# Kernel tuning notes

Measured on AMD Instinct MI355X. Metric: run time of the kernel, lower is better.

Reference implementation:

```python
import jax, jax.numpy as jnp
import numpy as np
import math

D = 2048
NH = 16       # query heads
NKV = 4       # kv heads (GQA)
HD = 128
SOFTCLAMP = 50.0
ROPE_BASE = 10000.0
B = 4
SQ_VLM = 1024
SQ_ACT = 64
S_CACHE = 256


def _heads(x, n):
    # [B,S,n*HD] -> [B,n,S,HD]
    b, s, _ = x.shape
    return x.reshape(b, s, n, HD).transpose(0, 2, 1, 3)


def _rope_cos_sin(pos):
    # pos: [B,S] int -> cos,sin [B,1,S,HD]
    inv_freq = 1.0 / (ROPE_BASE ** (jnp.arange(0, HD, 2, dtype=jnp.float32) / HD))
    freqs = pos.astype(jnp.float32)[..., None] * inv_freq  # [B,S,HD/2]
    emb = jnp.concatenate([freqs, freqs], axis=-1)         # [B,S,HD]
    return jnp.cos(emb)[:, None], jnp.sin(emb)[:, None]


def _apply_rope(x, cos, sin):
    # x: [B,H,S,HD]
    x1, x2 = x[..., : HD // 2], x[..., HD // 2 :]
    rot = jnp.concatenate([-x2, x1], axis=-1)
    return x * cos + rot * sin


def setup_inputs() -> dict:
    key = jax.random.key(0)
    ks = jax.random.split(key, 16)
    sc = lambda d: 1.0 / math.sqrt(d)
    inp = {
        'attention_mask': jnp.zeros((B, 1, SQ_VLM + SQ_ACT, S_CACHE + SQ_VLM + SQ_ACT), jnp.float32),
        'pos_vlm': jnp.broadcast_to(jnp.arange(S_CACHE, S_CACHE + SQ_VLM, dtype=jnp.int32), (B, SQ_VLM)),
        'pos_action': jnp.broadcast_to(jnp.arange(S_CACHE + SQ_VLM, S_CACHE + SQ_VLM + SQ_ACT, dtype=jnp.int32), (B, SQ_ACT)),
        'h_vlm': jax.random.normal(ks[0], (B, SQ_VLM, D), jnp.float32),
        'h_action': jax.random.normal(ks[1], (B, SQ_ACT, D), jnp.float32),
        'k_cache': jax.random.normal(ks[2], (B, NKV, S_CACHE, HD), jnp.float32),
        'v_cache': jax.random.normal(ks[3], (B, NKV, S_CACHE, HD), jnp.float32),
        'Wq_vlm': jax.random.normal(ks[4], (D, NH * HD), jnp.float32) * sc(D),
        'Wk_vlm': jax.random.normal(ks[5], (D, NKV * HD), jnp.float32) * sc(D),
        'Wv_vlm': jax.random.normal(ks[6], (D, NKV * HD), jnp.float32) * sc(D),
        'Wq_act': jax.random.normal(ks[7], (D, NH * HD), jnp.float32) * sc(D),
        'Wk_act': jax.random.normal(ks[8], (D, NKV * HD), jnp.float32) * sc(D),
        'Wv_act': jax.random.normal(ks[9], (D, NKV * HD), jnp.float32) * sc(D),
        'Wo_act': jax.random.normal(ks[10], (NH * HD, D), jnp.float32) * sc(NH * HD),
    }
    return inp


def reference(attention_mask, pos_vlm, pos_action, h_vlm, h_action, k_cache, v_cache,
              Wq_vlm, Wk_vlm, Wv_vlm, Wq_act, Wk_act, Wv_act, Wo_act):
    group = NH // NKV

    def qkv(h, pos, Wq, Wk, Wv):
        q = _heads(h @ Wq, NH)
        k = _heads(h @ Wk, NKV)
        v = _heads(h @ Wv, NKV)
        cos, sin = _rope_cos_sin(pos)
        return _apply_rope(q, cos, sin), _apply_rope(k, cos, sin), v

    q_v, k_v, v_v = qkv(h_vlm, pos_vlm, Wq_vlm, Wk_vlm, Wv_vlm)
    q_a, k_a, v_a = qkv(h_action, pos_action, Wq_act, Wk_act, Wv_act)

    # repeat_kv (GQA) on every KV source, cached mixture first (append_non_active order)
    rep = lambda t: jnp.repeat(t, group, axis=1)  # [B,NKV,S,HD] -> [B,NH,S,HD]
    k = jnp.concatenate([rep(k_cache), rep(k_v), rep(k_a)], axis=2)
    v = jnp.concatenate([rep(v_cache), rep(v_v), rep(v_a)], axis=2)
    q = jnp.concatenate([q_v, q_a], axis=2)  # [B,NH,Sq,HD]

    scores = jnp.einsum('bhqd,bhkd->bhqk', q, k) / math.sqrt(HD)
    scores = jnp.tanh(scores / SOFTCLAMP) * SOFTCLAMP + attention_mask
    w = jax.nn.softmax(scores.astype(jnp.float32), axis=-1).astype(q.dtype)
    out = jnp.einsum('bhqk,bhkd->bhqd', w, v)
    out = out.transpose(0, 2, 1, 3).reshape(B, SQ_VLM + SQ_ACT, NH * HD)

    # split by q_lens; 'vlm' is in post_attn_skip_names -> no o_proj, dropped
    out_action = out[:, SQ_VLM:, :]
    return out_action @ Wo_act
```

## Files before the change

### kernel.cpp

```cpp
#include <hip/hip_runtime.h>
#include <cmath>

#define NH 16
#define NKV 4
#define HD 128
#define DMODEL 2048
#define BB 4
#define SQV 1024
#define SQA 64
#define SCACHE 256
#define STOT 1344
#define SQTOT 1088
#define NSPLIT 7

typedef unsigned short u16;
typedef __attribute__((ext_vector_type(8))) short short8;
typedef __attribute__((ext_vector_type(4))) float f32x4;

__device__ __forceinline__ float b2f(u16 u) {
    union { float f; unsigned int i; } x; x.i = ((unsigned int)u) << 16; return x.f;
}
__device__ __forceinline__ u16 f2b(float f) {
    unsigned int x = __float_as_uint(f);
    x = x + 0x7fffu + ((x >> 16) & 1u);
    return (u16)(x >> 16);
}

__device__ __forceinline__ void gload16(const void* g, void* l) {
    __builtin_amdgcn_global_load_lds((const __attribute__((address_space(1))) void*)g,
                                     (__attribute__((address_space(3))) void*)l, 16, 0, 0);
}

__device__ __forceinline__ void transpose_body(const float* in, u16* out, int N,
                                               int bx, int by) {
    __shared__ __align__(16) u16 t[64 * 66];
    int n0 = bx * 64, k0 = by * 64;
    int tid = threadIdx.x;
    int r = tid >> 3;
    int c8 = (tid & 7) * 8;
#pragma unroll
    for (int h = 0; h < 2; h++) {
        int k = r + h * 32;
        const float* f = in + (size_t)(k0 + k) * N + n0 + c8;
        float4 a = *(const float4*)f, b = *(const float4*)(f + 4);
        u16 vv[8] = {f2b(a.x), f2b(a.y), f2b(a.z), f2b(a.w),
                     f2b(b.x), f2b(b.y), f2b(b.z), f2b(b.w)};
#pragma unroll
        for (int j = 0; j < 8; j++) t[(c8 + j) * 66 + k] = vv[j];
    }
    __syncthreads();
#pragma unroll
    for (int h = 0; h < 2; h++) {
        int n = r + h * 32;
        short8 v;
#pragma unroll
        for (int j = 0; j < 8; j++) ((u16*)&v)[j] = t[n * 66 + c8 + j];
        *(short8*)(out + (size_t)(n0 + n) * 2048 + k0 + c8) = v;
    }
}

__device__ __forceinline__ void transpose_vc(const float* vc, u16* VT, int idx) {
    __shared__ __align__(16) u16 tv[64 * 66];
    int bkv = idx >> 3, t8 = idx & 7;
    int key0 = (t8 >> 1) * 64, d0 = (t8 & 1) * 64;
    const float* in = vc + ((size_t)bkv * SCACHE + key0) * HD + d0;
    u16* out = VT + ((size_t)bkv * HD + d0) * STOT + key0;
    int tid = threadIdx.x;
    int r = tid >> 3, c8 = (tid & 7) * 8;
#pragma unroll
    for (int h = 0; h < 2; h++) {
        int k = r + h * 32;
        const float* f = in + (size_t)k * HD + c8;
        float4 a = *(const float4*)f, b = *(const float4*)(f + 4);
        u16 vv[8] = {f2b(a.x), f2b(a.y), f2b(a.z), f2b(a.w),
                     f2b(b.x), f2b(b.y), f2b(b.z), f2b(b.w)};
#pragma unroll
        for (int j = 0; j < 8; j++) tv[(c8 + j) * 66 + k] = vv[j];
    }
    __syncthreads();
#pragma unroll
    for (int h = 0; h < 2; h++) {
        int d = r + h * 32;
        short8 v;
#pragma unroll
        for (int j = 0; j < 8; j++) ((u16*)&v)[j] = tv[d * 66 + c8 + j];
        *(short8*)(out + (size_t)d * STOT + c8) = v;
    }
}

__global__ void k_prep(const float* __restrict__ mask,
                       const float* __restrict__ kc, const float* __restrict__ vc,
                       const float* __restrict__ hv, const float* __restrict__ ha,
                       const float* __restrict__ w0, u16* __restrict__ o0,
                       const float* __restrict__ w1, u16* __restrict__ o1,
                       const float* __restrict__ w2, u16* __restrict__ o2,
                       const float* __restrict__ w3, u16* __restrict__ o3,
                       const float* __restrict__ w4, u16* __restrict__ o4,
                       const float* __restrict__ w5, u16* __restrict__ o5,
                       float* __restrict__ cosT, float* __restrict__ sinT,
                       u16* __restrict__ maskS, u16* __restrict__ K_all, u16* __restrict__ VT_all,
                       u16* __restrict__ hv16, u16* __restrict__ ha16) {
    int gx = blockIdx.x, tid = threadIdx.x;
    if (gx < 3072) {
        if (gx < 256)        transpose_body(w0, o0, 512,  gx & 7,  gx >> 3);
        else if (gx < 512)   { int g = gx - 256;  transpose_body(w1, o1, 512,  g & 7,  g >> 3); }
        else if (gx < 768)   { int g = gx - 512;  transpose_body(w2, o2, 512,  g & 7,  g >> 3); }
        else if (gx < 1024)  { int g = gx - 768;  transpose_body(w3, o3, 512,  g & 7,  g >> 3); }
        else if (gx < 2048)  { int g = gx - 1024; transpose_body(w4, o4, 2048, g & 31, g >> 5); }
        else                 { int g = gx - 2048; transpose_body(w5, o5, 2048, g & 31, g >> 5); }
        return;
    }
    int bx = gx - 3072;
    if (bx < 336) {
        int i = bx * 256 + tid;
        if (i < STOT * 64) {
            int p = i >> 6, j = i & 63;
            float inv = __expf(-(float)j * (9.210340371976184f / 64.0f));
            float ang = (float)p * inv;
            cosT[i] = cosf(ang);
            sinT[i] = sinf(ang);
        }
    } else if (bx < 1680) {
        int i = (bx - 336) * 256 + tid;
        int b = i / (SQA * STOT);
        int r = i % (SQA * STOT);
        size_t s = (size_t)b * SQTOT * STOT + (size_t)SQV * STOT + r;
        maskS[i] = f2b(mask[s]);
    } else if (bx < 1936) {
        int i = (bx - 1680) * 256 + tid;
        int e = i * 8;
        int bk = e / (SCACHE * HD);
        int off = e % (SCACHE * HD);
        size_t dst = (size_t)bk * STOT * HD + off;
        const float* fk = kc + e;
        u16 tk[8];
#pragma unroll
        for (int j = 0; j < 8; j++) tk[j] = f2b(fk[j]);
        *(short8*)(K_all + dst) = *(short8*)tk;
    } else if (bx < 6032) {
        int i = (bx - 1936) * 256 + tid;
        int e = i * 8;
        const float* f = hv + e;
        float4 a = *(const float4*)f, b = *(const float4*)(f + 4);
        u16 t[8] = {f2b(a.x), f2b(a.y), f2b(a.z), f2b(a.w),
                    f2b(b.x), f2b(b.y), f2b(b.z), f2b(b.w)};
        *(short8*)(hv16 + e) = *(short8*)t;
    } else if (bx < 6288) {
        int i = (bx - 6032) * 256 + tid;
        int e = i * 8;
        const float* f = ha + e;
        float4 a = *(const float4*)f, b = *(const float4*)(f + 4);
        u16 t[8] = {f2b(a.x), f2b(a.y), f2b(a.z), f2b(a.w),
                    f2b(b.x), f2b(b.y), f2b(b.z), f2b(b.w)};
        *(short8*)(ha16 + e) = *(short8*)t;
    } else {
        transpose_vc(vc, VT_all, bx - 6288);
    }
}

__global__ __launch_bounds__(256) void k_gemm_qkv(
    const u16* __restrict__ Avlm, const u16* __restrict__ Aact,
    const u16* __restrict__ WkvT, const u16* __restrict__ WvvT,
    const u16* __restrict__ WqaT, const u16* __restrict__ WkaT, const u16* __restrict__ WvaT,
    const int* __restrict__ pos_vlm, const int* __restrict__ pos_act,
    const float* __restrict__ cosT, const float* __restrict__ sinT,
    u16* __restrict__ Qbuf, u16* __restrict__ K_all, u16* __restrict__ VT_all) {
    __shared__ __align__(16) u16 smem[2 * 16384];
    int tid = threadIdx.x;
    int w = tid >> 6, lane = tid & 63;
    int la = lane & 15, lg = lane >> 4;
    int wm = (w & 1) * 64;
    int c2 = w >> 1;
    int ntab[4] = {c2 * 2, c2 * 2 + 1, c2 * 2 + 4, c2 * 2 + 5};

    const u16* A; const u16* Bt; int m0, n0;
    int path;
    int head;
    int bid = blockIdx.x;
    if (bid < 256) {
        m0 = (bid & 31) * 128;
        int yy = bid >> 5;
        path = (yy < 4) ? 0 : 1;
        head = yy & 3;
        n0 = head * 128;
        A = Avlm;
        Bt = (path == 0) ? WkvT : WvvT;
    } else {
        int g = bid - 256;
        m0 = (g & 1) * 128;
        int ny = g >> 1;
        A = Aact;
        if (ny < 16)      { path = 2; head = ny;      Bt = WqaT; n0 = ny * 128; }
        else if (ny < 20) { path = 3; head = ny - 16; Bt = WkaT; n0 = (ny - 16) * 128; }
        else              { path = 4; head = ny - 20; Bt = WvaT; n0 = (ny - 20) * 128; }
    }

    f32x4 acc[4][4];
#pragma unroll
    for (int i = 0; i < 4; i++)
#pragma unroll
        for (int j = 0; j < 4; j++) acc[i][j] = (f32x4){0.f, 0.f, 0.f, 0.f};

    int srow = tid >> 3;
    int scsrc = (((tid & 7) * 16) ^ ((srow & 7) << 4)) >> 1;

#define STAGE_QKV(CB, KB) do {                                                        \
        u16* Ab_ = smem + (CB) * 16384;                                               \
        u16* Bb_ = Ab_ + 8192;                                                        \
        _Pragma("unroll")                                                             \
        for (int h = 0; h < 4; h++)                                                   \
            gload16(A + (size_t)(m0 + srow + h * 32) * DMODEL + (KB) + scsrc,         \
                    Ab_ + h * 2048 + tid * 8);                                        \
        _Pragma("unroll")                                                             \
        for (int h = 0; h < 4; h++)                                                   \
            gload16(Bt + (size_t)(n0 + srow + h * 32) * DMODEL + (KB) + scsrc,        \
                    Bb_ + h * 2048 + tid * 8);                                        \
    } while (0)

    STAGE_QKV(0, 0);
    int cur = 0;
    int swr = (la & 7) << 3;
    for (int kb = 0; kb < DMODEL; kb += 64) {
        if (kb + 64 < DMODEL) {
            STAGE_QKV(cur ^ 1, kb + 64);
            asm volatile("s_waitcnt vmcnt(8)" ::: "memory");
        } else {
            asm volatile("s_waitcnt vmcnt(0)" ::: "memory");
        }
        __builtin_amdgcn_s_barrier();
        asm volatile("" ::: "memory");
        const u16* Ac = smem + cur * 16384;
        const u16* Bc = Ac + 8192;
#pragma unroll
        for (int kk = 0; kk < 2; kk++) {
            short8 af[4], bf[4];
            int cc = (kk * 32 + lg * 8) ^ swr;
#pragma unroll
            for (int mt = 0; mt < 4; mt++)
                af[mt] = *(const short8*)&Ac[(wm + mt * 16 + la) * 64 + cc];
#pragma unroll
            for (int nt = 0; nt < 4; nt++)
                bf[nt] = *(const short8*)&Bc[(ntab[nt] * 16 + la) * 64 + cc];
#pragma unroll
            for (int mt = 0; mt < 4; mt++)
#pragma unroll
                for (int nt = 0; nt < 4; nt++)
                    acc[mt][nt] = __builtin_amdgcn_mfma_f32_16x16x32_bf16(af[mt], bf[nt], acc[mt][nt], 0, 0, 0);
        }
        __builtin_amdgcn_s_barrier();
        cur ^= 1;
    }
#undef STAGE_QKV

#pragma unroll
    for (int mt = 0; mt < 4; mt++) {
#pragma unroll
        for (int r = 0; r < 4; r++) {
            int gm = m0 + wm + mt * 16 + lg * 4 + r;
            if (path <= 1) {
                int b = gm >> 10, s = gm & 1023;
                if (path == 0) {
                    size_t base = ((size_t)(b * NKV + head) * STOT + SCACHE + s) * HD;
                    int pos = pos_vlm[gm];
#pragma unroll
                    for (int i = 0; i < 2; i++) {
                        int dlo = ntab[i] * 16 + la;
                        float x1 = acc[mt][i][r], x2 = acc[mt][i + 2][r];
                        float cs = cosT[pos * 64 + dlo], sn = sinT[pos * 64 + dlo];
                        K_all[base + dlo]      = f2b(x1 * cs - x2 * sn);
                        K_all[base + dlo + 64] = f2b(x2 * cs + x1 * sn);
                    }
                } else {
                    size_t vt = ((size_t)(b * NKV + head) * HD) * STOT + SCACHE + s;
#pragma unroll
                    for (int i = 0; i < 4; i++) {
                        int d = ntab[i] * 16 + la;
                        VT_all[vt + (size_t)d * STOT] = f2b(acc[mt][i][r]);
                    }
                }
            } else {
                int b = gm >> 6, s = gm & 63;
                if (path == 2) {
                    int pos = pos_act[gm];
                    size_t qb = ((size_t)(b * NH + head) * SQA + s) * HD;
#pragma unroll
                    for (int i = 0; i < 2; i++) {
                        int dlo = ntab[i] * 16 + la;
                        float x1 = acc[mt][i][r], x2 = acc[mt][i + 2][r];
                        float cs = cosT[pos * 64 + dlo], sn = sinT[pos * 64 + dlo];
                        Qbuf[qb + dlo]      = f2b(x1 * cs - x2 * sn);
                        Qbuf[qb + dlo + 64] = f2b(x2 * cs + x1 * sn);
                    }
                } else if (path == 3) {
                    int pos = pos_act[gm];
                    size_t base = ((size_t)(b * NKV + head) * STOT + SCACHE + SQV + s) * HD;
#pragma unroll
                    for (int i = 0; i < 2; i++) {
                        int dlo = ntab[i] * 16 + la;
                        float x1 = acc[mt][i][r], x2 = acc[mt][i + 2][r];
                        float cs = cosT[pos * 64 + dlo], sn = sinT[pos * 64 + dlo];
                        K_all[base + dlo]      = f2b(x1 * cs - x2 * sn);
                        K_all[base + dlo + 64] = f2b(x2 * cs + x1 * sn);
                    }
                } else {
                    size_t vt = ((size_t)(b * NKV + head) * HD) * STOT + SCACHE + SQV + s;
#pragma unroll
                    for (int i = 0; i < 4; i++) {
                        int d = ntab[i] * 16 + la;
                        VT_all[vt + (size_t)d * STOT] = f2b(acc[mt][i][r]);
                    }
                }
            }
        }
    }
}

__global__ __launch_bounds__(256) void k_attn_split(
    const u16* __restrict__ Qbuf, const u16* __restrict__ K_all, const u16* __restrict__ VT_all,
    const u16* __restrict__ maskS, u16* __restrict__ po, float* __restrict__ pml) {
    int h = blockIdx.x, b = blockIdx.y, p = blockIdx.z;
    int bh = b * NH + h;
    int kvh = h >> 2;
    const u16* Kb  = K_all  + (size_t)(b * NKV + kvh) * STOT * HD;
    const u16* VTb = VT_all + (size_t)(b * NKV + kvh) * HD * STOT;
    const u16* Qb  = Qbuf + (size_t)bh * SQA * HD;
    int tid = threadIdx.x, w = tid >> 6, lane = tid & 63;
    int la = lane & 15, lg = lane >> 4;
    __shared__ __align__(16) u16 Ks[2][64 * 128];
    __shared__ __align__(16) u16 Vt[2][128 * 64];
    __shared__ __align__(16) u16 Ps[4][16 * 72];
    short8 qf[4];
#pragma unroll
    for (int kk = 0; kk < 4; kk++)
        qf[kk] = *(const short8*)(Qb + (size_t)(w * 16 + la) * HD + kk * 32 + lg * 8);
    f32x4 o_acc[8];
#pragma unroll
    for (int nt = 0; nt < 8; nt++) o_acc[nt] = (f32x4){0.f, 0.f, 0.f, 0.f};
    float m_run[4], l_run[4];
#pragma unroll
    for (int r = 0; r < 4; r++) { m_run[r] = -3e38f; l_run[r] = 0.f; }

    int kr = tid >> 4;
    int ksw = (((tid & 15) * 16) ^ ((kr & 7) << 4)) >> 1;
    int vr = tid >> 3;
    int vsw = (((tid & 7) * 16) ^ ((vr & 7) << 4)) >> 1;

#define ASTAGE(CB, G) do {                                                            \
        _Pragma("unroll")                                                             \
        for (int hh = 0; hh < 4; hh++)                                                \
            gload16(Kb + (size_t)((G) * 64 + kr + hh * 16) * HD + ksw,                \
                    &Ks[CB][hh * 2048 + tid * 8]);                                    \
        _Pragma("unroll")                                                             \
        for (int hh = 0; hh < 4; hh++)                                                \
            gload16(VTb + (size_t)(vr + hh * 32) * STOT + (G) * 64 + vsw,             \
                    &Vt[CB][hh * 2048 + tid * 8]);                                    \
    } while (0)

    ASTAGE(0, p * 3);
    int cur = 0;
    int swr = (la & 7) << 3;
    const float scl = 0.08838834764831845f;
    for (int c = 0; c < 3; c++) {
        int g = p * 3 + c;
        u16 mreg[4][4];
#pragma unroll
        for (int nt = 0; nt < 4; nt++)
#pragma unroll
            for (int r = 0; r < 4; r++)
                mreg[nt][r] = maskS[((size_t)(b * SQA + w * 16 + lg * 4 + r)) * STOT +
                                    g * 64 + nt * 16 + la];
        if (c < 2) {
            ASTAGE(cur ^ 1, g + 1);
            asm volatile("s_waitcnt vmcnt(8)" ::: "memory");
        } else {
            asm volatile("s_waitcnt vmcnt(0)" ::: "memory");
        }
        __builtin_amdgcn_s_barrier();
        asm volatile("" ::: "memory");
        f32x4 s_acc[4];
#pragma unroll
        for (int nt = 0; nt < 4; nt++) s_acc[nt] = (f32x4){0.f, 0.f, 0.f, 0.f};
        __builtin_amdgcn_s_setprio(1);
#pragma unroll
        for (int kk = 0; kk < 4; kk++) {
            int cc = (kk * 32 + lg * 8) ^ swr;
#pragma unroll
            for (int nt = 0; nt < 4; nt++) {
                short8 kf = *(const short8*)&Ks[cur][(nt * 16 + la) * 128 + cc];
                s_acc[nt] = __builtin_amdgcn_mfma_f32_16x16x32_bf16(qf[kk], kf, s_acc[nt], 0, 0, 0);
            }
        }
        __builtin_amdgcn_s_setprio(0);
        float sc[4][4];
#pragma unroll
        for (int nt = 0; nt < 4; nt++) {
#pragma unroll
            for (int r = 0; r < 4; r++) {
                float sv = s_acc[nt][r] * scl;
                float x = sv * 0.02f;
                float t = __expf(-2.0f * fabsf(x));
                float th = __fdividef(1.0f - t, 1.0f + t);
                sv = copysignf(th, x) * 50.0f;
                sv += b2f(mreg[nt][r]);
                sc[nt][r] = sv;
            }
        }
#pragma unroll
        for (int r = 0; r < 4; r++) {
            float mx = fmaxf(fmaxf(sc[0][r], sc[1][r]), fmaxf(sc[2][r], sc[3][r]));
#pragma unroll
            for (int sh = 1; sh < 16; sh <<= 1) mx = fmaxf(mx, __shfl_xor(mx, sh, 64));
            float mn = fmaxf(m_run[r], mx);
            float alpha = __expf(m_run[r] - mn);
            m_run[r] = mn;
            float rowsum = 0.f;
#pragma unroll
            for (int nt = 0; nt < 4; nt++) {
                float pv = __expf(sc[nt][r] - mn);
                Ps[w][(lg * 4 + r) * 72 + nt * 16 + la] = f2b(pv);
                rowsum += pv;
            }
#pragma unroll
            for (int sh = 1; sh < 16; sh <<= 1) rowsum += __shfl_xor(rowsum, sh, 64);
            l_run[r] = l_run[r] * alpha + rowsum;
#pragma unroll
            for (int nt = 0; nt < 8; nt++) o_acc[nt][r] *= alpha;
        }
        __builtin_amdgcn_s_setprio(1);
#pragma unroll
        for (int kk = 0; kk < 2; kk++) {
            short8 pf = *(const short8*)&Ps[w][la * 72 + kk * 32 + lg * 8];
            int cc = (kk * 32 + lg * 8) ^ swr;
#pragma unroll
            for (int nt = 0; nt < 8; nt++) {
                short8 vf = *(const short8*)&Vt[cur][(nt * 16 + la) * 64 + cc];
                o_acc[nt] = __builtin_amdgcn_mfma_f32_16x16x32_bf16(pf, vf, o_acc[nt], 0, 0, 0);
            }
        }
        __builtin_amdgcn_s_setprio(0);
        __builtin_amdgcn_s_barrier();
        cur ^= 1;
    }
#undef ASTAGE
#pragma unroll
    for (int nt = 0; nt < 8; nt++) {
#pragma unroll
        for (int r = 0; r < 4; r++) {
            int sq = w * 16 + lg * 4 + r;
            po[(((size_t)p * 64 + bh) * 64 + sq) * 128 + nt * 16 + la] = f2b(o_acc[nt][r]);
        }
    }
    if (la == 0) {
#pragma unroll
        for (int r = 0; r < 4; r++) {
            int sq = w * 16 + lg * 4 + r;
            size_t mlb = (((size_t)p * 64 + bh) * 64 + sq) * 2;
            pml[mlb] = m_run[r];
            pml[mlb + 1] = l_run[r];
        }
    }
}

__global__ __launch_bounds__(256) void k_attn_red(
    const u16* __restrict__ po, const float* __restrict__ pml, u16* __restrict__ AO) {
    int h = blockIdx.x, b = blockIdx.y;
    int bh = b * NH + h;
    __shared__ float wgt[NSPLIT][64];
    int tid = threadIdx.x;
    if (tid < 64) {
        int q = tid;
        float m[NSPLIT], l[NSPLIT], M = -3e38f;
#pragma unroll
        for (int p = 0; p < NSPLIT; p++) {
            size_t mlb = (((size_t)p * 64 + bh) * 64 + q) * 2;
            m[p] = pml[mlb]; l[p] = pml[mlb + 1];
            M = fmaxf(M, m[p]);
        }
        float L = 0.f;
#pragma unroll
        for (int p = 0; p < NSPLIT; p++) L += l[p] * __expf(m[p] - M);
        float inv = 1.0f / L;
#pragma unroll
        for (int p = 0; p < NSPLIT; p++) wgt[p][q] = __expf(m[p] - M) * inv;
    }
    __syncthreads();
    for (int e = tid; e < 64 * 128; e += 256) {
        int q = e >> 7, d = e & 127;
        float s = 0.f;
#pragma unroll
        for (int p = 0; p < NSPLIT; p++)
            s += b2f(po[(((size_t)p * 64 + bh) * 64 + q) * 128 + d]) * wgt[p][q];
        AO[((size_t)(b * SQA + q)) * 2048 + h * HD + d] = f2b(s);
    }
}

__global__ __launch_bounds__(256) void k_gemm_out(
    const u16* __restrict__ A, const u16* __restrict__ WoT, float* __restrict__ out) {
    __shared__ __align__(16) u16 smem[2 * 8192];
    int m0 = blockIdx.x * 64, n0 = blockIdx.y * 64;
    int tid = threadIdx.x;
    int w = tid >> 6, lane = tid & 63;
    int la = lane & 15, lg = lane >> 4;
    int wm = (w & 1) * 32, wn = (w >> 1) * 32;
    f32x4 acc[2][2];
#pragma unroll
    for (int i = 0; i < 2; i++)
#pragma unroll
        for (int j = 0; j < 2; j++) acc[i][j] = (f32x4){0.f, 0.f, 0.f, 0.f};

    int srow = tid >> 3;
    int scsrc = (((tid & 7) * 16) ^ ((srow & 7) << 4)) >> 1;

#define STAGE_OUT(CB, KB) do {                                                        \
        u16* Ab_ = smem + (CB) * 8192;                                                \
        u16* Bb_ = Ab_ + 4096;                                                        \
        _Pragma("unroll")                                                             \
        for (int h = 0; h < 2; h++)                                                   \
            gload16(A + (size_t)(m0 + srow + h * 32) * DMODEL + (KB) + scsrc,         \
                    Ab_ + h * 2048 + w * 512);                                        \
        _Pragma("unroll")                                                             \
        for (int h = 0; h < 2; h++)                                                   \
            gload16(WoT + (size_t)(n0 + srow + h * 32) * DMODEL + (KB) + scsrc,       \
                    Bb_ + h * 2048 + w * 512);                                        \
    } while (0)

    STAGE_OUT(0, 0);
    int cur = 0;
    int swr = (la & 7) << 3;
    for (int kb = 0; kb < DMODEL; kb += 64) {
        if (kb + 64 < DMODEL) {
            STAGE_OUT(cur ^ 1, kb + 64);
            asm volatile("s_waitcnt vmcnt(4)" ::: "memory");
        } else {
            asm volatile("s_waitcnt vmcnt(0)" ::: "memory");
        }
        __builtin_amdgcn_s_barrier();
        asm volatile("" ::: "memory");
        const u16* Ac = smem + cur * 8192;
        const u16* Bc = Ac + 4096;
#pragma unroll
        for (int kk = 0; kk < 2; kk++) {
            short8 af[2], bf[2];
            int cc = (kk * 32 + lg * 8) ^ swr;
#pragma unroll
            for (int mt = 0; mt < 2; mt++) af[mt] = *(const short8*)&Ac[(wm + mt * 16 + la) * 64 + cc];
#pragma unroll
            for (int nt = 0; nt < 2; nt++) bf[nt] = *(const short8*)&Bc[(wn + nt * 16 + la) * 64 + cc];
#pragma unroll
            for (int mt = 0; mt < 2; mt++)
#pragma unroll
                for (int nt = 0; nt < 2; nt++)
                    acc[mt][nt] = __builtin_amdgcn_mfma_f32_16x16x32_bf16(af[mt], bf[nt], acc[mt][nt], 0, 0, 0);
        }
        __builtin_amdgcn_s_barrier();
        cur ^= 1;
    }
#undef STAGE_OUT

#pragma unroll
    for (int mt = 0; mt < 2; mt++) {
#pragma unroll
        for (int r = 0; r < 4; r++) {
            int gm = m0 + wm + mt * 16 + lg * 4 + r;
#pragma unroll
            for (int nt = 0; nt < 2; nt++)
                out[(size_t)gm * DMODEL + n0 + wn + nt * 16 + la] = acc[mt][nt][r];
        }
    }
}

extern "C" void kernel_launch(void* const* d_in, const int* in_sizes, int n_in,
                              void* d_out, int out_size, void* d_ws, size_t ws_size,
                              hipStream_t stream) {
    (void)in_sizes; (void)n_in; (void)out_size;
    const float* mask    = (const float*)d_in[0];
    const int*   pos_vlm = (const int*)d_in[1];
    const int*   pos_act = (const int*)d_in[2];
    const float* h_vlm   = (const float*)d_in[3];
    const float* h_act   = (const float*)d_in[4];
    const float* k_cache = (const float*)d_in[5];
    const float* v_cache = (const float*)d_in[6];
    const float* Wk_vlm  = (const float*)d_in[8];
    const float* Wv_vlm  = (const float*)d_in[9];
    const float* Wq_act  = (const float*)d_in[10];
    const float* Wk_act  = (const float*)d_in[11];
    const float* Wv_act  = (const float*)d_in[12];
    const float* Wo_act  = (const float*)d_in[13];

    const size_t NEED = 65273856;
    if (ws_size < NEED) return;
    char* ws = (char*)d_ws;
    float* cosT  = (float*)(ws + 0);
    float* sinT  = (float*)(ws + 344064);
    u16* K_all   = (u16*)(ws + 688128);
    u16* VT_all  = (u16*)(ws + 6193152);
    u16* Qbuf    = (u16*)(ws + 11698176);
    u16* AO      = (u16*)(ws + 12746752);
    u16* WkvT    = (u16*)(ws + 13795328);
    u16* WvvT    = (u16*)(ws + 15892480);
    u16* WqaT    = (u16*)(ws + 17989632);
    u16* WkaT    = (u16*)(ws + 26378240);
    u16* WvaT    = (u16*)(ws + 28475392);
    u16* WoT     = (u16*)(ws + 30572544);
    u16* po      = (u16*)(ws + 38961152);
    float* pml   = (float*)(ws + 46301184);
    u16* maskS   = (u16*)(ws + 46759936);
    u16* hv16    = (u16*)(ws + 47448064);
    u16* ha16    = (u16*)(ws + 64225280);

    hipLaunchKernelGGL(k_prep, dim3(9488), dim3(256), 0, stream,
                       mask, k_cache, v_cache, h_vlm, h_act,
                       Wk_vlm, WkvT, Wv_vlm, WvvT, Wk_act, WkaT, Wv_act, WvaT,
                       Wq_act, WqaT, Wo_act, WoT,
                       cosT, sinT, maskS, K_all, VT_all, hv16, ha16);
    hipLaunchKernelGGL(k_gemm_qkv, dim3(304), dim3(256), 0, stream,
                       hv16, ha16, WkvT, WvvT, WqaT, WkaT, WvaT,
                       pos_vlm, pos_act, cosT, sinT, Qbuf, K_all, VT_all);
    hipLaunchKernelGGL(k_attn_split, dim3(16, 4, NSPLIT), dim3(256), 0, stream,
                       Qbuf, K_all, VT_all, maskS, po, pml);
    hipLaunchKernelGGL(k_attn_red, dim3(16, 4), dim3(256), 0, stream, po, pml, AO);
    hipLaunchKernelGGL(k_gemm_out, dim3(4, 32), dim3(256), 0, stream, AO, WoT, (float*)d_out);
}
```

Measured before the change: 233.6 us.

## Shrink tiles and raise split count to fill more compute units across kernels

```diff
diff --git a/kernel.cpp b/kernel.cpp
--- a/kernel.cpp
+++ b/kernel.cpp
@@ -11,7 +11,7 @@
 #define SCACHE 256
 #define STOT 1344
 #define SQTOT 1088
-#define NSPLIT 7
+#define NSPLIT 21
 
 typedef unsigned short u16;
 typedef __attribute__((ext_vector_type(8))) short short8;
@@ -165,11 +165,11 @@
     const int* __restrict__ pos_vlm, const int* __restrict__ pos_act,
     const float* __restrict__ cosT, const float* __restrict__ sinT,
     u16* __restrict__ Qbuf, u16* __restrict__ K_all, u16* __restrict__ VT_all) {
-    __shared__ __align__(16) u16 smem[2 * 16384];
+    __shared__ __align__(16) u16 smem[2 * 12288];
     int tid = threadIdx.x;
     int w = tid >> 6, lane = tid & 63;
     int la = lane & 15, lg = lane >> 4;
-    int wm = (w & 1) * 64;
+    int wm = (w & 1) * 32;
     int c2 = w >> 1;
     int ntab[4] = {c2 * 2, c2 * 2 + 1, c2 * 2 + 4, c2 * 2 + 5};
 
@@ -177,27 +177,27 @@
     int path;
     int head;
     int bid = blockIdx.x;
-    if (bid < 256) {
-        m0 = (bid & 31) * 128;
-        int yy = bid >> 5;
+    if (bid < 512) {
+        m0 = (bid & 63) * 64;
+        int yy = bid >> 6;
         path = (yy < 4) ? 0 : 1;
         head = yy & 3;
         n0 = head * 128;
         A = Avlm;
         Bt = (path == 0) ? WkvT : WvvT;
     } else {
-        int g = bid - 256;
-        m0 = (g & 1) * 128;
-        int ny = g >> 1;
+        int g = bid - 512;
+        m0 = (g & 3) * 64;
+        int ny = g >> 2;
         A = Aact;
         if (ny < 16)      { path = 2; head = ny;      Bt = WqaT; n0 = ny * 128; }
         else if (ny < 20) { path = 3; head = ny - 16; Bt = WkaT; n0 = (ny - 16) * 128; }
         else              { path = 4; head = ny - 20; Bt = WvaT; n0 = (ny - 20) * 128; }
     }
 
-    f32x4 acc[4][4];
-#pragma unroll
-    for (int i = 0; i < 4; i++)
+    f32x4 acc[2][4];
+#pragma unroll
+    for (int i = 0; i < 2; i++)
 #pragma unroll
         for (int j = 0; j < 4; j++) acc[i][j] = (f32x4){0.f, 0.f, 0.f, 0.f};
 
@@ -205,10 +205,10 @@
     int scsrc = (((tid & 7) * 16) ^ ((srow & 7) << 4)) >> 1;
 
 #define STAGE_QKV(CB, KB) do {                                                        \
-        u16* Ab_ = smem + (CB) * 16384;                                               \
-        u16* Bb_ = Ab_ + 8192;                                                        \
+        u16* Ab_ = smem + (CB) * 12288;                                               \
+        u16* Bb_ = Ab_ + 4096;                                                        \
         _Pragma("unroll")                                                             \
-        for (int h = 0; h < 4; h++)                                                   \
+        for (int h = 0; h < 2; h++)                                                   \
             gload16(A + (size_t)(m0 + srow + h * 32) * DMODEL + (KB) + scsrc,         \
                     Ab_ + h * 2048 + tid * 8);                                        \
         _Pragma("unroll")                                                             \
@@ -223,26 +223,26 @@
     for (int kb = 0; kb < DMODEL; kb += 64) {
         if (kb + 64 < DMODEL) {
             STAGE_QKV(cur ^ 1, kb + 64);
-            asm volatile("s_waitcnt vmcnt(8)" ::: "memory");
+            asm volatile("s_waitcnt vmcnt(6)" ::: "memory");
         } else {
             asm volatile("s_waitcnt vmcnt(0)" ::: "memory");
         }
         __builtin_amdgcn_s_barrier();
         asm volatile("" ::: "memory");
-        const u16* Ac = smem + cur * 16384;
-        const u16* Bc = Ac + 8192;
+        const u16* Ac = smem + cur * 12288;
+        const u16* Bc = Ac + 4096;
 #pragma unroll
         for (int kk = 0; kk < 2; kk++) {
-            short8 af[4], bf[4];
+            short8 af[2], bf[4];
             int cc = (kk * 32 + lg * 8) ^ swr;
 #pragma unroll
-            for (int mt = 0; mt < 4; mt++)
+            for (int mt = 0; mt < 2; mt++)
                 af[mt] = *(const short8*)&Ac[(wm + mt * 16 + la) * 64 + cc];
 #pragma unroll
             for (int nt = 0; nt < 4; nt++)
                 bf[nt] = *(const short8*)&Bc[(ntab[nt] * 16 + la) * 64 + cc];
 #pragma unroll
-            for (int mt = 0; mt < 4; mt++)
+            for (int mt = 0; mt < 2; mt++)
 #pragma unroll
                 for (int nt = 0; nt < 4; nt++)
                     acc[mt][nt] = __builtin_amdgcn_mfma_f32_16x16x32_bf16(af[mt], bf[nt], acc[mt][nt], 0, 0, 0);
@@ -253,7 +253,7 @@
 #undef STAGE_QKV
 
 #pragma unroll
-    for (int mt = 0; mt < 4; mt++) {
+    for (int mt = 0; mt < 2; mt++) {
 #pragma unroll
         for (int r = 0; r < 4; r++) {
             int gm = m0 + wm + mt * 16 + lg * 4 + r;
@@ -326,122 +326,100 @@
     const u16* Qb  = Qbuf + (size_t)bh * SQA * HD;
     int tid = threadIdx.x, w = tid >> 6, lane = tid & 63;
     int la = lane & 15, lg = lane >> 4;
-    __shared__ __align__(16) u16 Ks[2][64 * 128];
-    __shared__ __align__(16) u16 Vt[2][128 * 64];
+    __shared__ __align__(16) u16 Ks[64 * 128];
+    __shared__ __align__(16) u16 Vt[128 * 64];
     __shared__ __align__(16) u16 Ps[4][16 * 72];
-    short8 qf[4];
-#pragma unroll
-    for (int kk = 0; kk < 4; kk++)
-        qf[kk] = *(const short8*)(Qb + (size_t)(w * 16 + la) * HD + kk * 32 + lg * 8);
-    f32x4 o_acc[8];
-#pragma unroll
-    for (int nt = 0; nt < 8; nt++) o_acc[nt] = (f32x4){0.f, 0.f, 0.f, 0.f};
-    float m_run[4], l_run[4];
-#pragma unroll
-    for (int r = 0; r < 4; r++) { m_run[r] = -3e38f; l_run[r] = 0.f; }
 
     int kr = tid >> 4;
     int ksw = (((tid & 15) * 16) ^ ((kr & 7) << 4)) >> 1;
     int vr = tid >> 3;
     int vsw = (((tid & 7) * 16) ^ ((vr & 7) << 4)) >> 1;
-
-#define ASTAGE(CB, G) do {                                                            \
-        _Pragma("unroll")                                                             \
-        for (int hh = 0; hh < 4; hh++)                                                \
-            gload16(Kb + (size_t)((G) * 64 + kr + hh * 16) * HD + ksw,                \
-                    &Ks[CB][hh * 2048 + tid * 8]);                                    \
-        _Pragma("unroll")                                                             \
-        for (int hh = 0; hh < 4; hh++)                                                \
-            gload16(VTb + (size_t)(vr + hh * 32) * STOT + (G) * 64 + vsw,             \
-                    &Vt[CB][hh * 2048 + tid * 8]);                                    \
-    } while (0)
-
-    ASTAGE(0, p * 3);
-    int cur = 0;
+#pragma unroll
+    for (int hh = 0; hh < 4; hh++)
+        gload16(Kb + (size_t)(p * 64 + kr + hh * 16) * HD + ksw, &Ks[hh * 2048 + tid * 8]);
+#pragma unroll
+    for (int hh = 0; hh < 4; hh++)
+        gload16(VTb + (size_t)(vr + hh * 32) * STOT + p * 64 + vsw, &Vt[hh * 2048 + tid * 8]);
+
+    short8 qf[4];
+#pragma unroll
+    for (int kk = 0; kk < 4; kk++)
+        qf[kk] = *(const short8*)(Qb + (size_t)(w * 16 + la) * HD + kk * 32 + lg * 8);
+    u16 mreg[4][4];
+#pragma unroll
+    for (int nt = 0; nt < 4; nt++)
+#pragma unroll
+        for (int r = 0; r < 4; r++)
+            mreg[nt][r] = maskS[((size_t)(b * SQA + w * 16 + lg * 4 + r)) * STOT +
+                                p * 64 + nt * 16 + la];
+
+    asm volatile("s_waitcnt vmcnt(0)" ::: "memory");
+    __builtin_amdgcn_s_barrier();
+    asm volatile("" ::: "memory");
+
     int swr = (la & 7) << 3;
     const float scl = 0.08838834764831845f;
-    for (int c = 0; c < 3; c++) {
-        int g = p * 3 + c;
-        u16 mreg[4][4];
-#pragma unroll
-        for (int nt = 0; nt < 4; nt++)
-#pragma unroll
-            for (int r = 0; r < 4; r++)
-                mreg[nt][r] = maskS[((size_t)(b * SQA + w * 16 + lg * 4 + r)) * STOT +
-                                    g * 64 + nt * 16 + la];
-        if (c < 2) {
-            ASTAGE(cur ^ 1, g + 1);
-            asm volatile("s_waitcnt vmcnt(8)" ::: "memory");
-        } else {
-            asm volatile("s_waitcnt vmcnt(0)" ::: "memory");
-        }
-        __builtin_amdgcn_s_barrier();
-        asm volatile("" ::: "memory");
-        f32x4 s_acc[4];
-#pragma unroll
-        for (int nt = 0; nt < 4; nt++) s_acc[nt] = (f32x4){0.f, 0.f, 0.f, 0.f};
-        __builtin_amdgcn_s_setprio(1);
-#pragma unroll
-        for (int kk = 0; kk < 4; kk++) {
-            int cc = (kk * 32 + lg * 8) ^ swr;
-#pragma unroll
-            for (int nt = 0; nt < 4; nt++) {
-                short8 kf = *(const short8*)&Ks[cur][(nt * 16 + la) * 128 + cc];
-                s_acc[nt] = __builtin_amdgcn_mfma_f32_16x16x32_bf16(qf[kk], kf, s_acc[nt], 0, 0, 0);
-            }
-        }
-        __builtin_amdgcn_s_setprio(0);
-        float sc[4][4];
+    f32x4 s_acc[4];
+#pragma unroll
+    for (int nt = 0; nt < 4; nt++) s_acc[nt] = (f32x4){0.f, 0.f, 0.f, 0.f};
+    __builtin_amdgcn_s_setprio(1);
+#pragma unroll
+    for (int kk = 0; kk < 4; kk++) {
+        int cc = (kk * 32 + lg * 8) ^ swr;
 #pragma unroll
         for (int nt = 0; nt < 4; nt++) {
-#pragma unroll
-            for (int r = 0; r < 4; r++) {
-                float sv = s_acc[nt][r] * scl;
-                float x = sv * 0.02f;
-                float t = __expf(-2.0f * fabsf(x));
-                float th = __fdividef(1.0f - t, 1.0f + t);
-                sv = copysignf(th, x) * 50.0f;
-                sv += b2f(mreg[nt][r]);
-                sc[nt][r] = sv;
-            }
-        }
+            short8 kf = *(const short8*)&Ks[(nt * 16 + la) * 128 + cc];
+            s_acc[nt] = __builtin_amdgcn_mfma_f32_16x16x32_bf16(qf[kk], kf, s_acc[nt], 0, 0, 0);
+        }
+    }
+    __builtin_amdgcn_s_setprio(0);
+    float sc[4][4];
+#pragma unroll
+    for (int nt = 0; nt < 4; nt++) {
 #pragma unroll
         for (int r = 0; r < 4; r++) {
-            float mx = fmaxf(fmaxf(sc[0][r], sc[1][r]), fmaxf(sc[2][r], sc[3][r]));
-#pragma unroll
-            for (int sh = 1; sh < 16; sh <<= 1) mx = fmaxf(mx, __shfl_xor(mx, sh, 64));
-            float mn = fmaxf(m_run[r], mx);
-            float alpha = __expf(m_run[r] - mn);
-            m_run[r] = mn;
-            float rowsum = 0.f;
-#pragma unroll
-            for (int nt = 0; nt < 4; nt++) {
-                float pv = __expf(sc[nt][r] - mn);
-                Ps[w][(lg * 4 + r) * 72 + nt * 16 + la] = f2b(pv);
-                rowsum += pv;
-            }
-#pragma unroll
-            for (int sh = 1; sh < 16; sh <<= 1) rowsum += __shfl_xor(rowsum, sh, 64);
-            l_run[r] = l_run[r] * alpha + rowsum;
-#pragma unroll
-            for (int nt = 0; nt < 8; nt++) o_acc[nt][r] *= alpha;
-        }
-        __builtin_amdgcn_s_setprio(1);
-#pragma unroll
-        for (int kk = 0; kk < 2; kk++) {
-            short8 pf = *(const short8*)&Ps[w][la * 72 + kk * 32 + lg * 8];
-            int cc = (kk * 32 + lg * 8) ^ swr;
-#pragma unroll
-            for (int nt = 0; nt < 8; nt++) {
-                short8 vf = *(const short8*)&Vt[cur][(nt * 16 + la) * 64 + cc];
-                o_acc[nt] = __builtin_amdgcn_mfma_f32_16x16x32_bf16(pf, vf, o_acc[nt], 0, 0, 0);
-            }
-        }
-        __builtin_amdgcn_s_setprio(0);
-        __builtin_amdgcn_s_barrier();
-        cur ^= 1;
-    }
-#undef ASTAGE
+            float sv = s_acc[nt][r] * scl;
+            float x = sv * 0.02f;
+            float t = __expf(-2.0f * fabsf(x));
+            float th = __fdividef(1.0f - t, 1.0f + t);
+            sv = copysignf(th, x) * 50.0f;
+            sv += b2f(mreg[nt][r]);
+            sc[nt][r] = sv;
+        }
+    }
+    float m_fin[4], l_fin[4];
+#pragma unroll
+    for (int r = 0; r < 4; r++) {
+        float mx = fmaxf(fmaxf(sc[0][r], sc[1][r]), fmaxf(sc[2][r], sc[3][r]));
+#pragma unroll
+        for (int sh = 1; sh < 16; sh <<= 1) mx = fmaxf(mx, __shfl_xor(mx, sh, 64));
+        float rowsum = 0.f;
+#pragma unroll
+        for (int nt = 0; nt < 4; nt++) {
+            float pv = __expf(sc[nt][r] - mx);
+            Ps[w][(lg * 4 + r) * 72 + nt * 16 + la] = f2b(pv);
+            rowsum += pv;
+        }
+#pragma unroll
+        for (int sh = 1; sh < 16; sh <<= 1) rowsum += __shfl_xor(rowsum, sh, 64);
+        m_fin[r] = mx;
+        l_fin[r] = rowsum;
+    }
+    f32x4 o_acc[8];
+#pragma unroll
+    for (int nt = 0; nt < 8; nt++) o_acc[nt] = (f32x4){0.f, 0.f, 0.f, 0.f};
+    __builtin_amdgcn_s_setprio(1);
+#pragma unroll
+    for (int kk = 0; kk < 2; kk++) {
+        short8 pf = *(const short8*)&Ps[w][la * 72 + kk * 32 + lg * 8];
+        int cc = (kk * 32 + lg * 8) ^ swr;
+#pragma unroll
+        for (int nt = 0; nt < 8; nt++) {
+            short8 vf = *(const short8*)&Vt[(nt * 16 + la) * 64 + cc];
+            o_acc[nt] = __builtin_amdgcn_mfma_f32_16x16x32_bf16(pf, vf, o_acc[nt], 0, 0, 0);
+        }
+    }
+    __builtin_amdgcn_s_setprio(0);
 #pragma unroll
     for (int nt = 0; nt < 8; nt++) {
 #pragma unroll
@@ -455,20 +433,20 @@
         for (int r = 0; r < 4; r++) {
             int sq = w * 16 + lg * 4 + r;
             size_t mlb = (((size_t)p * 64 + bh) * 64 + sq) * 2;
-            pml[mlb] = m_run[r];
-            pml[mlb + 1] = l_run[r];
+            pml[mlb] = m_fin[r];
+            pml[mlb + 1] = l_fin[r];
         }
     }
 }
 
 __global__ __launch_bounds__(256) void k_attn_red(
     const u16* __restrict__ po, const float* __restrict__ pml, u16* __restrict__ AO) {
-    int h = blockIdx.x, b = blockIdx.y;
+    int h = blockIdx.x, b = blockIdx.y, qz = blockIdx.z * 16;
     int bh = b * NH + h;
-    __shared__ float wgt[NSPLIT][64];
+    __shared__ float wgt[NSPLIT][16];
     int tid = threadIdx.x;
-    if (tid < 64) {
-        int q = tid;
+    if (tid < 16) {
+        int q = qz + tid;
         float m[NSPLIT], l[NSPLIT], M = -3e38f;
 #pragma unroll
         for (int p = 0; p < NSPLIT; p++) {
@@ -481,47 +459,42 @@
         for (int p = 0; p < NSPLIT; p++) L += l[p] * __expf(m[p] - M);
         float inv = 1.0f / L;
 #pragma unroll
-        for (int p = 0; p < NSPLIT; p++) wgt[p][q] = __expf(m[p] - M) * inv;
+        for (int p = 0; p < NSPLIT; p++) wgt[p][tid] = __expf(m[p] - M) * inv;
     }
     __syncthreads();
-    for (int e = tid; e < 64 * 128; e += 256) {
-        int q = e >> 7, d = e & 127;
+    for (int e = tid; e < 16 * 128; e += 256) {
+        int q = qz + (e >> 7), d = e & 127;
         float s = 0.f;
 #pragma unroll
         for (int p = 0; p < NSPLIT; p++)
-            s += b2f(po[(((size_t)p * 64 + bh) * 64 + q) * 128 + d]) * wgt[p][q];
+            s += b2f(po[(((size_t)p * 64 + bh) * 64 + q) * 128 + d]) * wgt[p][e >> 7];
         AO[((size_t)(b * SQA + q)) * 2048 + h * HD + d] = f2b(s);
     }
 }
 
 __global__ __launch_bounds__(256) void k_gemm_out(
     const u16* __restrict__ A, const u16* __restrict__ WoT, float* __restrict__ out) {
-    __shared__ __align__(16) u16 smem[2 * 8192];
-    int m0 = blockIdx.x * 64, n0 = blockIdx.y * 64;
+    __shared__ __align__(16) u16 smem[2 * 6144];
+    int m0 = blockIdx.x * 32, n0 = blockIdx.y * 64;
     int tid = threadIdx.x;
     int w = tid >> 6, lane = tid & 63;
     int la = lane & 15, lg = lane >> 4;
-    int wm = (w & 1) * 32, wn = (w >> 1) * 32;
-    f32x4 acc[2][2];
-#pragma unroll
-    for (int i = 0; i < 2; i++)
-#pragma unroll
-        for (int j = 0; j < 2; j++) acc[i][j] = (f32x4){0.f, 0.f, 0.f, 0.f};
+    int wm = (w & 1) * 16, wn = (w >> 1) * 32;
+    f32x4 acc[2];
+#pragma unroll
+    for (int j = 0; j < 2; j++) acc[j] = (f32x4){0.f, 0.f, 0.f, 0.f};
 
     int srow = tid >> 3;
     int scsrc = (((tid & 7) * 16) ^ ((srow & 7) << 4)) >> 1;
 
 #define STAGE_OUT(CB, KB) do {                                                        \
-        u16* Ab_ = smem + (CB) * 8192;                                                \
-        u16* Bb_ = Ab_ + 4096;                                                        \
-        _Pragma("unroll")                                                             \
-        for (int h = 0; h < 2; h++)                                                   \
-            gload16(A + (size_t)(m0 + srow + h * 32) * DMODEL + (KB) + scsrc,         \
-                    Ab_ + h * 2048 + w * 512);                                        \
+        u16* Ab_ = smem + (CB) * 6144;                                                \
+        u16* Bb_ = Ab_ + 2048;                                                        \
+        gload16(A + (size_t)(m0 + srow) * DMODEL + (KB) + scsrc, Ab_ + tid * 8);      \
         _Pragma("unroll")                                                             \
         for (int h = 0; h < 2; h++)                                                   \
             gload16(WoT + (size_t)(n0 + srow + h * 32) * DMODEL + (KB) + scsrc,       \
-                    Bb_ + h * 2048 + w * 512);                                        \
+                    Bb_ + h * 2048 + tid * 8);                                        \
     } while (0)
 
     STAGE_OUT(0, 0);
@@ -530,27 +503,24 @@
     for (int kb = 0; kb < DMODEL; kb += 64) {
         if (kb + 64 < DMODEL) {
             STAGE_OUT(cur ^ 1, kb + 64);
-            asm volatile("s_waitcnt vmcnt(4)" ::: "memory");
+            asm volatile("s_waitcnt vmcnt(3)" ::: "memory");
         } else {
             asm volatile("s_waitcnt vmcnt(0)" ::: "memory");
         }
         __builtin_amdgcn_s_barrier();
         asm volatile("" ::: "memory");
-        const u16* Ac = smem + cur * 8192;
-        const u16* Bc = Ac + 4096;
+        const u16* Ac = smem + cur * 6144;
+        const u16* Bc = Ac + 2048;
 #pragma unroll
         for (int kk = 0; kk < 2; kk++) {
-            short8 af[2], bf[2];
             int cc = (kk * 32 + lg * 8) ^ swr;
-#pragma unroll
-            for (int mt = 0; mt < 2; mt++) af[mt] = *(const short8*)&Ac[(wm + mt * 16 + la) * 64 + cc];
+            short8 af = *(const short8*)&Ac[(wm + la) * 64 + cc];
+            short8 bf[2];
 #pragma unroll
             for (int nt = 0; nt < 2; nt++) bf[nt] = *(const short8*)&Bc[(wn + nt * 16 + la) * 64 + cc];
 #pragma unroll
-            for (int mt = 0; mt < 2; mt++)
-#pragma unroll
-                for (int nt = 0; nt < 2; nt++)
-                    acc[mt][nt] = __builtin_amdgcn_mfma_f32_16x16x32_bf16(af[mt], bf[nt], acc[mt][nt], 0, 0, 0);
+            for (int nt = 0; nt < 2; nt++)
+                acc[nt] = __builtin_amdgcn_mfma_f32_16x16x32_bf16(af, bf[nt], acc[nt], 0, 0, 0);
         }
         __builtin_amdgcn_s_barrier();
         cur ^= 1;
@@ -558,14 +528,11 @@
 #undef STAGE_OUT
 
 #pragma unroll
-    for (int mt = 0; mt < 2; mt++) {
-#pragma unroll
-        for (int r = 0; r < 4; r++) {
-            int gm = m0 + wm + mt * 16 + lg * 4 + r;
-#pragma unroll
-            for (int nt = 0; nt < 2; nt++)
-                out[(size_t)gm * DMODEL + n0 + wn + nt * 16 + la] = acc[mt][nt][r];
-        }
+    for (int r = 0; r < 4; r++) {
+        int gm = m0 + wm + lg * 4 + r;
+#pragma unroll
+        for (int nt = 0; nt < 2; nt++)
+            out[(size_t)gm * DMODEL + n0 + wn + nt * 16 + la] = acc[nt][r];
     }
 }
 
@@ -587,7 +554,7 @@
     const float* Wv_act  = (const float*)d_in[12];
     const float* Wo_act  = (const float*)d_in[13];
 
-    const size_t NEED = 65273856;
+    const size_t NEED = 80183296;
     if (ws_size < NEED) return;
     char* ws = (char*)d_ws;
     float* cosT  = (float*)(ws + 0);
@@ -603,21 +570,21 @@
     u16* WvaT    = (u16*)(ws + 28475392);
     u16* WoT     = (u16*)(ws + 30572544);
     u16* po      = (u16*)(ws + 38961152);
-    float* pml   = (float*)(ws + 46301184);
-    u16* maskS   = (u16*)(ws + 46759936);
-    u16* hv16    = (u16*)(ws + 47448064);
-    u16* ha16    = (u16*)(ws + 64225280);
+    float* pml   = (float*)(ws + 60981248);
+    u16* maskS   = (u16*)(ws + 61669376);
+    u16* hv16    = (u16*)(ws + 62357504);
+    u16* ha16    = (u16*)(ws + 79134720);
 
     hipLaunchKernelGGL(k_prep, dim3(9488), dim3(256), 0, stream,
                        mask, k_cache, v_cache, h_vlm, h_act,
                        Wk_vlm, WkvT, Wv_vlm, WvvT, Wk_act, WkaT, Wv_act, WvaT,
                        Wq_act, WqaT, Wo_act, WoT,
                        cosT, sinT, maskS, K_all, VT_all, hv16, ha16);
-    hipLaunchKernelGGL(k_gemm_qkv, dim3(304), dim3(256), 0, stream,
+    hipLaunchKernelGGL(k_gemm_qkv, dim3(608), dim3(256), 0, stream,
                        hv16, ha16, WkvT, WvvT, WqaT, WkaT, WvaT,
                        pos_vlm, pos_act, cosT, sinT, Qbuf, K_all, VT_all);
     hipLaunchKernelGGL(k_attn_split, dim3(16, 4, NSPLIT), dim3(256), 0, stream,
                        Qbuf, K_all, VT_all, maskS, po, pml);
-    hipLaunchKernelGGL(k_attn_red, dim3(16, 4), dim3(256), 0, stream, po, pml, AO);
-    hipLaunchKernelGGL(k_gemm_out, dim3(4, 32), dim3(256), 0, stream, AO, WoT, (float*)d_out);
-}
+    hipLaunchKernelGGL(k_attn_red, dim3(16, 4, 4), dim3(256), 0, stream, po, pml, AO);
+    hipLaunchKernelGGL(k_gemm_out, dim3(8, 32), dim3(256), 0, stream, AO, WoT, (float*)d_out);
+}
```

Measured after the change: 232.7 us. About the same (-0.4%).
